# Kernel optimization log

Hardware: AMD Instinct MI355X
Metric: run time of the kernel (lower is better)

## Reference

```python
import jax, jax.numpy as jnp
import numpy as np

B, T, V, E, H, C = 128, 200, 50000, 300, 512, 3

def _lstm_scan(x, W_ih, W_hh, b_ih, b_hh, h0, c0):
    # x: [B,T,E]; torch LSTMCell gate order: i, f, g, o
    xg = jnp.einsum('bte,ge->btg', x, W_ih) + b_ih + b_hh  # [B,T,4H]
    def step(carry, xg_t):
        h, c = carry
        gates = xg_t + h @ W_hh.T
        i, f, g, o = jnp.split(gates, 4, axis=-1)
        c = jax.nn.sigmoid(f) * c + jax.nn.sigmoid(i) * jnp.tanh(g)
        h = jax.nn.sigmoid(o) * jnp.tanh(c)
        return (h, c), (h, c)
    _, (hs, cs) = jax.lax.scan(step, (h0, c0), jnp.swapaxes(xg, 0, 1))
    return hs, cs  # [T,B,H]

def _mask_blend(hs, cs, m, h0, c0):
    # hs,cs: [T,B,H]; m: [T,B]; carry-forward previous state where mask==0
    def step(carry, inp):
        h_p, c_p = carry
        h_t, c_t, m_t = inp
        m_t = m_t[:, None]
        h_p = m_t * h_t + (1.0 - m_t) * h_p
        c_p = m_t * c_t + (1.0 - m_t) * c_p
        return (h_p, c_p), (h_p, c_p)
    _, (mh, mc) = jax.lax.scan(step, (h0, c0), (hs, cs, m))
    return mh, mc

def setup_inputs() -> dict:
    key = jax.random.key(0)
    ks = jax.random.split(key, 12)
    s_e = 1.0 / np.sqrt(H)
    u = lambda k, shp: jax.random.uniform(k, shp, jnp.float32, -s_e, s_e)
    return {
        'premise': jax.random.randint(ks[0], (B, T), 0, V),
        'hypothesis': jax.random.randint(ks[1], (B, T), 0, V),
        'similarity': jax.random.uniform(ks[2], (B, 1), jnp.float32),
        'emb_weight': jax.random.normal(ks[3], (V, E), jnp.float32),
        'Wih_p': u(ks[4], (4 * H, E)), 'Whh_p': u(ks[5], (4 * H, H)),
        'bih_p': u(ks[6], (4 * H,)), 'bhh_p': u(ks[7], (4 * H,)),
        'Wih_h': u(ks[8], (4 * H, E)), 'Whh_h': u(ks[9], (4 * H, H)),
        'bih_h': u(ks[10], (4 * H,)), 'bhh_h': u(ks[11], (4 * H,)),
        'fc_W': jax.random.normal(jax.random.fold_in(key, 100), (C, H + 1), jnp.float32) * 0.02,
        'fc_b': jnp.zeros((C,), jnp.float32),
    }

def reference(premise, hypothesis, similarity, emb_weight,
              Wih_p, Whh_p, bih_p, bhh_p, Wih_h, Whh_h, bih_h, bhh_h,
              fc_W, fc_b):
    emb_p = emb_weight[premise]            # [B,T,E]
    emb_h = emb_weight[hypothesis]
    mask_p = (premise != 0).astype(jnp.float32).T   # [T,B]
    mask_h = (hypothesis != 0).astype(jnp.float32).T
    h0 = jnp.zeros((B, H), jnp.float32)
    c0 = jnp.zeros((B, H), jnp.float32)
    # premise LSTM (raw, unmasked recurrence as in original)
    hs_p, cs_p = _lstm_scan(emb_p, Wih_p, Whh_p, bih_p, bhh_p, h0, c0)
    _, mc_p = _mask_blend(hs_p, cs_p, mask_p, h0, c0)
    c_last = mc_p[-1]                      # masked last premise cell
    # hypothesis LSTM: hidden reset, cell carried
    hs_h, cs_h = _lstm_scan(emb_h, Wih_h, Whh_h, bih_h, bhh_h, h0, c_last)
    mh_h, _ = _mask_blend(hs_h, cs_h, mask_h, h0, c_last)
    feat = jnp.concatenate([mh_h[-1], similarity], axis=1)  # [B,H+1]
    logits = feat @ fc_W.T + fc_b
    # dropout inactive (eval mode)
    return jax.nn.log_softmax(logits, axis=1)
```

## Files before the change

kernel.cpp:

```cpp
#include <hip/hip_runtime.h>
#include <hip/hip_bf16.h>

#define B_ 128
#define T_ 200
#define H_ 512
#define G_ 2048
#define E_ 300

typedef unsigned short u16;
typedef unsigned int u32;

using f32x4 = __attribute__((ext_vector_type(4))) float;
using s16x8 = __attribute__((ext_vector_type(8))) short;

__device__ __forceinline__ u16 f2bf(float f) {
  u32 u = __builtin_bit_cast(u32, f);
  u32 r = (u + 0x7fffu + ((u >> 16) & 1u)) >> 16;
  return (u16)r;
}
__device__ __forceinline__ float bf2f(u16 s) {
  return __builtin_bit_cast(float, (u32)s << 16);
}

__device__ __forceinline__ s16x8 ld_h16_sc(const void* p) {
  s16x8 r;
  asm volatile("global_load_dwordx4 %0, %1, off sc0 sc1" : "=v"(r) : "v"(p));
  return r;
}
__device__ __forceinline__ void st_h_sc(void* p, u32 v) {
  asm volatile("global_store_short %0, %1, off sc0 sc1" :: "v"(p), "v"(v));
}
__device__ __forceinline__ u32 ld_flag_sc(const void* p) {
  u32 r;
  asm volatile("global_load_dword %0, %1, off sc0 sc1\n\ts_waitcnt vmcnt(0)"
               : "=v"(r) : "v"(p) : "memory");
  return r;
}
__device__ __forceinline__ void st_flag_sc(void* p, u32 v) {
  asm volatile("global_store_dword %0, %1, off sc0 sc1" :: "v"(p), "v"(v) : "memory");
}

__global__ __launch_bounds__(64) void mask_k(
    const int* __restrict__ tok, u32* __restrict__ mb)
{
  const int idx = blockIdx.x * 64 + threadIdx.x;
  if (idx >= T_ * 4) return;
  const int t = idx >> 2, w = idx & 3;
  u32 bits = 0;
  for (int i = 0; i < 32; ++i)
    bits |= (tok[(w * 32 + i) * T_ + t] != 0 ? 1u : 0u) << i;
  mb[idx] = bits;
}

template<int TRACK_C>
__global__ __launch_bounds__(512, 2) void lstm_rec(
    const int* __restrict__ tok, const float* __restrict__ emb,
    const float* __restrict__ Wih, const float* __restrict__ bih,
    const float* __restrict__ bhh, const float* __restrict__ Whh,
    u16* __restrict__ hbuf, const float* __restrict__ c0in,
    float* __restrict__ cOut, float* __restrict__ mhOut,
    u32* __restrict__ flags, const u32* __restrict__ maskb)
{
  __shared__ f32x4 red[8][4][64];
  __shared__ f32x4 xr[2][4][64];
  const int tid = threadIdx.x;
  const int wv = tid >> 6, ln = tid & 63, lr = ln & 15, lq = ln >> 4;
  const int grp = (int)blockIdx.x >> 5, jt = (int)blockIdx.x & 31;
  const int j0 = jt * 16, bg0 = grp * 16;
  u32* gflags = flags + grp * 512;

  s16x8 Bf[4][2];
#pragma unroll
  for (int q = 0; q < 4; ++q) {
    const float* wr = Whh + (size_t)(q * H_ + j0 + lr) * H_ + wv * 64 + lq * 8;
#pragma unroll
    for (int ks = 0; ks < 2; ++ks) {
      const float* wp = wr + ks * 32;
      s16x8 f;
#pragma unroll
      for (int i = 0; i < 8; ++i) f[i] = (short)f2bf(wp[i]);
      Bf[q][ks] = f;
    }
  }

  const int qq = wv - 4;
  s16x8 Wf[10];
  if (wv >= 4) {
    const float* wr = Wih + (size_t)(qq * H_ + j0 + lr) * E_;
#pragma unroll
    for (int ks = 0; ks < 10; ++ks) {
      s16x8 f;
#pragma unroll
      for (int i = 0; i < 8; ++i) {
        const int k = ks * 32 + lq * 8 + i;
        f[i] = (short)((k < E_) ? f2bf(wr[k]) : (u16)0);
      }
      Wf[ks] = f;
    }
  }

  float c[4], mb[4], bias[4];
#pragma unroll
  for (int r = 0; r < 4; ++r) {
    const int b = bg0 + lq * 4 + r;
    float cv = 0.f;
    if (!TRACK_C && wv == 0) cv = c0in[b * H_ + j0 + lr];
    c[r] = cv;
    mb[r] = TRACK_C ? cv : 0.f;
  }
  if (wv == 0) {
#pragma unroll
    for (int q = 0; q < 4; ++q) {
      const int g = q * H_ + j0 + lr;
      bias[q] = bih[g] + bhh[g];
    }
  }

  if (wv >= 4) {
    const int tk = tok[(bg0 + lr) * T_ + 0];
    const float* er = emb + (size_t)tk * E_;
    f32x4 xacc = {0.f, 0.f, 0.f, 0.f};
#pragma unroll
    for (int ks = 0; ks < 10; ++ks) {
      s16x8 af;
#pragma unroll
      for (int i = 0; i < 8; ++i) {
        const int k = ks * 32 + lq * 8 + i;
        af[i] = (short)((k < E_) ? f2bf(er[k]) : (u16)0);
      }
      xacc = __builtin_amdgcn_mfma_f32_16x16x32_bf16(af, Wf[ks], xacc, 0, 0, 0);
    }
    xr[0][qq][ln] = xacc;
  }
  __syncthreads();

  const u32* pp = gflags + (ln & 31) * 16;
  const int mword = grp >> 1, mshift = (grp & 1) * 16;

  for (int t = 0; t < T_; ++t) {
    const u16* hrd = hbuf + (t & 1) * (B_ * H_);
    u16* hwr = hbuf + ((t + 1) & 1) * (B_ * H_);

    u32 mku = 0;
    if (wv == 0) {
      mku = maskb[t * 4 + mword] >> mshift;
      if (t > 0) {
        int guard = 0;
        for (;;) {
          u32 v = ld_flag_sc(pp);
          if (__all((int)(v >= (u32)t))) break;
          if (++guard > (1 << 22)) break;
          __builtin_amdgcn_s_sleep(1);
        }
      }
    } else if (wv >= 4 && t + 1 < T_) {
      const int tk = tok[(bg0 + lr) * T_ + (t + 1)];
      const float* er = emb + (size_t)tk * E_;
      f32x4 xacc = {0.f, 0.f, 0.f, 0.f};
#pragma unroll
      for (int ks = 0; ks < 10; ++ks) {
        s16x8 af;
#pragma unroll
        for (int i = 0; i < 8; ++i) {
          const int k = ks * 32 + lq * 8 + i;
          af[i] = (short)((k < E_) ? f2bf(er[k]) : (u16)0);
        }
        xacc = __builtin_amdgcn_mfma_f32_16x16x32_bf16(af, Wf[ks], xacc, 0, 0, 0);
      }
      xr[(t + 1) & 1][qq][ln] = xacc;
    }
    __syncthreads();
    __builtin_amdgcn_sched_barrier(0);

    s16x8 ha0, ha1;
    const u16* hb = hrd + (size_t)(bg0 + lr) * H_ + wv * 64 + lq * 8;
    ha0 = ld_h16_sc(hb);
    ha1 = ld_h16_sc(hb + 32);
    asm volatile("s_waitcnt vmcnt(0)" ::: "memory");
    __builtin_amdgcn_sched_barrier(0);

    f32x4 acc[4];
#pragma unroll
    for (int q = 0; q < 4; ++q) {
      acc[q] = __builtin_amdgcn_mfma_f32_16x16x32_bf16(ha0, Bf[q][0],
                   (f32x4){0.f, 0.f, 0.f, 0.f}, 0, 0, 0);
      acc[q] = __builtin_amdgcn_mfma_f32_16x16x32_bf16(ha1, Bf[q][1], acc[q], 0, 0, 0);
    }

    if (wv > 0) {
#pragma unroll
      for (int q = 0; q < 4; ++q) red[wv][q][ln] = acc[q];
    }
    __syncthreads();
    if (wv == 0) {
#pragma unroll
      for (int kv = 1; kv < 8; ++kv)
#pragma unroll
        for (int q = 0; q < 4; ++q) acc[q] += red[kv][q][ln];
      f32x4 xv[4];
#pragma unroll
      for (int q = 0; q < 4; ++q) xv[q] = xr[t & 1][q][ln];
      const bool last = (t == T_ - 1);
#pragma unroll
      for (int r = 0; r < 4; ++r) {
        const int b = bg0 + lq * 4 + r;
        const float gi = acc[0][r] + xv[0][r] + bias[0];
        const float gf = acc[1][r] + xv[1][r] + bias[1];
        const float gG = acc[2][r] + xv[2][r] + bias[2];
        const float go = acc[3][r] + xv[3][r] + bias[3];
        const float si = 1.f / (1.f + __expf(-gi));
        const float sf = 1.f / (1.f + __expf(-gf));
        const float so = 1.f / (1.f + __expf(-go));
        const float tg = 2.f / (1.f + __expf(-2.f * gG)) - 1.f;
        const float cn = sf * c[r] + si * tg;
        const float tc = 2.f / (1.f + __expf(-2.f * cn)) - 1.f;
        const float hn = so * tc;
        c[r] = cn;
        if ((mku >> (lq * 4 + r)) & 1u) mb[r] = TRACK_C ? cn : hn;
        if (!last) st_h_sc(hwr + (size_t)b * H_ + j0 + lr, (u32)f2bf(hn));
      }
      if (t + 1 < T_) {
        asm volatile("s_waitcnt vmcnt(0)" ::: "memory");
        if (ln == 0) st_flag_sc(gflags + jt * 16, (u32)(t + 1));
      }
    }
    __syncthreads();
  }

  if (wv == 0) {
#pragma unroll
    for (int r = 0; r < 4; ++r) {
      const int b = bg0 + lq * 4 + r;
      if (TRACK_C) cOut[b * H_ + j0 + lr] = mb[r];
      else         mhOut[b * H_ + j0 + lr] = mb[r];
    }
  }
}

__global__ __launch_bounds__(128) void final_k(
    const float* __restrict__ mh, const float* __restrict__ sim,
    const float* __restrict__ fcW, const float* __restrict__ fcb,
    float* __restrict__ out)
{
  const int b = threadIdx.x;
  float l[3];
#pragma unroll
  for (int cc = 0; cc < 3; ++cc) {
    const float* wr = fcW + cc * (H_ + 1);
    float s = fcb[cc] + sim[b] * wr[H_];
    for (int j = 0; j < H_; ++j) s += mh[b * H_ + j] * wr[j];
    l[cc] = s;
  }
  const float m = fmaxf(l[0], fmaxf(l[1], l[2]));
  const float lse = m + logf(__expf(l[0] - m) + __expf(l[1] - m) + __expf(l[2] - m));
  out[b * 3 + 0] = l[0] - lse;
  out[b * 3 + 1] = l[1] - lse;
  out[b * 3 + 2] = l[2] - lse;
}

extern "C" void kernel_launch(void* const* d_in, const int* in_sizes, int n_in,
                              void* d_out, int out_size, void* d_ws, size_t ws_size,
                              hipStream_t stream) {
  const int*   prem = (const int*)d_in[0];
  const int*   hypo = (const int*)d_in[1];
  const float* sim  = (const float*)d_in[2];
  const float* emb  = (const float*)d_in[3];
  const float* WihP = (const float*)d_in[4];
  const float* WhhP = (const float*)d_in[5];
  const float* bihP = (const float*)d_in[6];
  const float* bhhP = (const float*)d_in[7];
  const float* WihH = (const float*)d_in[8];
  const float* WhhH = (const float*)d_in[9];
  const float* bihH = (const float*)d_in[10];
  const float* bhhH = (const float*)d_in[11];
  const float* fcW  = (const float*)d_in[12];
  const float* fcb  = (const float*)d_in[13];
  float* out = (float*)d_out;

  char* ws = (char*)d_ws;
  const size_t HB_OFF = 0;
  const size_t CL_OFF = HB_OFF + (size_t)2 * B_ * H_ * 2;
  const size_t MH_OFF = CL_OFF + (size_t)B_ * H_ * 4;
  const size_t FL_OFF = MH_OFF + (size_t)B_ * H_ * 4;
  const size_t MK_OFF = FL_OFF + 32768;
  const size_t NEED   = MK_OFF + 8192;
  if (ws_size < NEED) return;

  u16*   hbuf  = (u16*)(ws + HB_OFF);
  float* cLast = (float*)(ws + CL_OFF);
  float* mh    = (float*)(ws + MH_OFF);
  u32*   flagsP = (u32*)(ws + FL_OFF);
  u32*   flagsH = flagsP + 4096;
  u32*   maskbP = (u32*)(ws + MK_OFF);
  u32*   maskbH = maskbP + 1024;

  hipMemsetAsync(ws + FL_OFF, 0, 32768, stream);

  mask_k<<<13, 64, 0, stream>>>(prem, maskbP);
  mask_k<<<13, 64, 0, stream>>>(hypo, maskbH);
  hipMemsetAsync(hbuf, 0, (size_t)B_ * H_ * 2, stream);
  lstm_rec<1><<<256, 512, 0, stream>>>(prem, emb, WihP, bihP, bhhP, WhhP,
                                       hbuf, nullptr, cLast, nullptr,
                                       flagsP, maskbP);
  hipMemsetAsync(hbuf, 0, (size_t)B_ * H_ * 2, stream);
  lstm_rec<0><<<256, 512, 0, stream>>>(hypo, emb, WihH, bihH, bhhH, WhhH,
                                       hbuf, cLast, nullptr, mh,
                                       flagsH, maskbH);
  final_k<<<1, 128, 0, stream>>>(mh, sim, fcW, fcb, out);
}
```

Measured before the change: 2.058 ms.

## Stage embedding rows in swizzled LDS and split gather from input-projection MFMA

Waves 1-2 now gather the next timestep's embedding rows with vectorized float4 loads, convert them to bf16 and write them into a swizzled shared buffer. Waves 4-7 later read MFMA operands from that buffer, and the input-projection MFMA moves to after the recurrent gate phase of each step. Before, each of waves 4-7 gathered scalar global loads redundantly before the barrier. The aim is to take the slow gather off the critical path before the barrier and cut redundant global traffic. The cost is extra LDS and a stage-to-stage dependency that relies on the existing barriers.

```diff
diff --git a/kernel.cpp b/kernel.cpp
--- a/kernel.cpp
+++ b/kernel.cpp
@@ -63,6 +63,7 @@
 {
   __shared__ f32x4 red[8][4][64];
   __shared__ f32x4 xr[2][4][64];
+  __shared__ u16 araw[16 * 320];
   const int tid = threadIdx.x;
   const int wv = tid >> 6, ln = tid & 63, lr = ln & 15, lq = ln >> 4;
   const int grp = (int)blockIdx.x >> 5, jt = (int)blockIdx.x & 31;
@@ -116,18 +117,29 @@
     }
   }
 
+  const int sidx = (wv - 1) * 64 + ln;
+  const int srow = sidx & 15, spart = sidx >> 4;
+  char* sdst = (char*)araw + srow * 640;
+  const int sswz = (srow & 7) << 4;
+
+  if (wv == 1 || wv == 2) {
+    const float* er = emb + (size_t)tok[(bg0 + srow) * T_ + 0] * E_;
+#pragma unroll
+    for (int ch = 0; ch < 10; ++ch) {
+      const int k = spart * 40 + ch * 4;
+      f32x4 v = (k + 4 <= E_) ? *(const f32x4*)(er + k) : (f32x4){0.f,0.f,0.f,0.f};
+      *(u32*)(sdst + ((k * 2) ^ sswz))     = (u32)f2bf(v[0]) | ((u32)f2bf(v[1]) << 16);
+      *(u32*)(sdst + ((k * 2 + 4) ^ sswz)) = (u32)f2bf(v[2]) | ((u32)f2bf(v[3]) << 16);
+    }
+  }
+  __syncthreads();
   if (wv >= 4) {
-    const int tk = tok[(bg0 + lr) * T_ + 0];
-    const float* er = emb + (size_t)tk * E_;
+    const char* abase = (const char*)araw + lr * 640;
+    const int aswz = (lr & 7) << 4;
     f32x4 xacc = {0.f, 0.f, 0.f, 0.f};
 #pragma unroll
     for (int ks = 0; ks < 10; ++ks) {
-      s16x8 af;
-#pragma unroll
-      for (int i = 0; i < 8; ++i) {
-        const int k = ks * 32 + lq * 8 + i;
-        af[i] = (short)((k < E_) ? f2bf(er[k]) : (u16)0);
-      }
+      s16x8 af = *(const s16x8*)(abase + ((ks * 64 + lq * 16) ^ aswz));
       xacc = __builtin_amdgcn_mfma_f32_16x16x32_bf16(af, Wf[ks], xacc, 0, 0, 0);
     }
     xr[0][qq][ln] = xacc;
@@ -153,21 +165,15 @@
           __builtin_amdgcn_s_sleep(1);
         }
       }
-    } else if (wv >= 4 && t + 1 < T_) {
-      const int tk = tok[(bg0 + lr) * T_ + (t + 1)];
-      const float* er = emb + (size_t)tk * E_;
-      f32x4 xacc = {0.f, 0.f, 0.f, 0.f};
-#pragma unroll
-      for (int ks = 0; ks < 10; ++ks) {
-        s16x8 af;
-#pragma unroll
-        for (int i = 0; i < 8; ++i) {
-          const int k = ks * 32 + lq * 8 + i;
-          af[i] = (short)((k < E_) ? f2bf(er[k]) : (u16)0);
-        }
-        xacc = __builtin_amdgcn_mfma_f32_16x16x32_bf16(af, Wf[ks], xacc, 0, 0, 0);
-      }
-      xr[(t + 1) & 1][qq][ln] = xacc;
+    } else if ((wv == 1 || wv == 2) && t + 1 < T_) {
+      const float* er = emb + (size_t)tok[(bg0 + srow) * T_ + (t + 1)] * E_;
+#pragma unroll
+      for (int ch = 0; ch < 10; ++ch) {
+        const int k = spart * 40 + ch * 4;
+        f32x4 v = (k + 4 <= E_) ? *(const f32x4*)(er + k) : (f32x4){0.f,0.f,0.f,0.f};
+        *(u32*)(sdst + ((k * 2) ^ sswz))     = (u32)f2bf(v[0]) | ((u32)f2bf(v[1]) << 16);
+        *(u32*)(sdst + ((k * 2 + 4) ^ sswz)) = (u32)f2bf(v[2]) | ((u32)f2bf(v[3]) << 16);
+      }
     }
     __syncthreads();
     __builtin_amdgcn_sched_barrier(0);
@@ -223,6 +229,16 @@
         asm volatile("s_waitcnt vmcnt(0)" ::: "memory");
         if (ln == 0) st_flag_sc(gflags + jt * 16, (u32)(t + 1));
       }
+    } else if (wv >= 4 && t + 1 < T_) {
+      const char* abase = (const char*)araw + lr * 640;
+      const int aswz = (lr & 7) << 4;
+      f32x4 xacc = {0.f, 0.f, 0.f, 0.f};
+#pragma unroll
+      for (int ks = 0; ks < 10; ++ks) {
+        s16x8 af = *(const s16x8*)(abase + ((ks * 64 + lq * 16) ^ aswz));
+        xacc = __builtin_amdgcn_mfma_f32_16x16x32_bf16(af, Wf[ks], xacc, 0, 0, 0);
+      }
+      xr[(t + 1) & 1][qq][ln] = xacc;
     }
     __syncthreads();
   }
```

Measured after the change: 2.098 ms. No clear change (+1.9%).
